# Optimization experiments

Measured on AMD Instinct MI355X. Metric: run time of the kernel, lower is better.

The kernel has to match this reference:

```python
import jax, jax.numpy as jnp
import numpy as np
import math

N0 = 50000      # nodes at level 0
E0 = 800000     # edges at level 0 (fixed edge buffer, masked when pooled)
D = 128         # hidden_dim == latent_dim
L = 2           # args.mpl_layers
NB = 2          # args.num_blocks (SAGEConvs per block)
RATIO = 0.5     # args.mpl_ratio
EPS = 1e-12


def setup_inputs() -> dict:
    key = jax.random.key(0)
    ks = jax.random.split(key, 6)
    x = jax.random.normal(ks[0], (N0, D), jnp.float32)
    edge_index = jax.random.randint(ks[1], (2, E0), 0, N0, jnp.int32)
    n_convs = (2 * L + 1) * NB  # down(4) + bottom(2) + up(4) = 10
    Wl = jax.random.normal(ks[2], (n_convs, D, D), jnp.float32) * 0.05
    bl = jax.random.normal(ks[3], (n_convs, D), jnp.float32) * 0.05
    Wr = jax.random.normal(ks[4], (n_convs, D, D), jnp.float32) * 0.05
    pool_p = jax.random.normal(ks[5], (L, D), jnp.float32)
    return {"x": x, "edge_index": edge_index, "Wl": Wl, "bl": bl, "Wr": Wr,
            "pool_p": pool_p}


def _sage(x, src, dst, valid, W_l, b_l, W_r, n):
    """PyG SAGEConv (mean aggr): lin_l(mean_{j->i} x_j) + lin_r(x_i).
    Invalid (masked) edges contribute neither to the sum nor the count."""
    msg = x[src] * valid[:, None]                       # [E, D]
    s = jax.ops.segment_sum(msg, dst, num_segments=n)   # [n, D]
    cnt = jax.ops.segment_sum(valid, dst, num_segments=n)
    mean = s / jnp.maximum(cnt, 1.0)[:, None]
    return mean @ W_l.T + b_l + x @ W_r.T


def _cal_ew(w, src, dst, valid, n):
    """WeightedEdgeConv.cal_ew (no_grad in original)."""
    deg = jax.ops.segment_sum(valid, src, num_segments=n)
    normed = w / jnp.where(deg > 0, deg, 1.0)
    w_send = normed[src] * valid
    aggr_w = jax.ops.segment_sum(w_send, dst, num_segments=n) + EPS
    ec = w_send / aggr_w[dst]
    return jax.lax.stop_gradient(ec), jax.lax.stop_gradient(aggr_w)


def _econv(x, src, dst, ec, n, aggregating=True):
    """WeightedEdgeConv.forward: gather -> scale by edge weight -> scatter-add."""
    if aggregating:
        return jax.ops.segment_sum(x[src] * ec[:, None], dst, num_segments=n)
    return jax.ops.segment_sum(x[dst] * ec[:, None], src, num_segments=n)


def reference(x, edge_index, Wl, bl, Wr, pool_p):
    src, dst = edge_index[0], edge_index[1]
    valid = jnp.ones((E0,), x.dtype)
    n = N0
    conv = 0
    down_outs, down_edges, ecs, perms, sizes = [], [], [], [], []
    w = jnp.ones((N0,), x.dtype)  # b_data.weights (ones by default)

    # ---- down path ----
    for l in range(L):
        for _ in range(NB):
            x = _sage(x, src, dst, valid, Wl[conv], bl[conv], Wr[conv], n)
            conv += 1
        down_outs.append(x)
        down_edges.append((src, dst, valid))
        sizes.append(n)
        ec, w = _cal_ew(w, src, dst, valid, n)
        ecs.append(ec)
        x = _econv(x, src, dst, ec, n, aggregating=True)
        # TopKPooling: score = x.p/||p||, keep top ceil(ratio*n), gate by tanh
        p = pool_p[l]
        score = x @ p / jnp.linalg.norm(p)
        k = int(math.ceil(RATIO * n))
        vals, perm = jax.lax.top_k(score, k)
        x = x[perm] * jnp.tanh(vals)[:, None]
        w = w[perm]
        new_id = jnp.full((n,), -1, jnp.int32).at[perm].set(
            jnp.arange(k, dtype=jnp.int32))
        src2, dst2 = new_id[src], new_id[dst]
        keep = ((src2 >= 0) & (dst2 >= 0)).astype(x.dtype)
        valid = valid * keep
        src = jnp.maximum(src2, 0)
        dst = jnp.maximum(dst2, 0)
        perms.append(perm)
        n = k

    # ---- bottom ----
    for _ in range(NB):
        x = _sage(x, src, dst, valid, Wl[conv], bl[conv], Wr[conv], n)
        conv += 1

    # ---- up path ----
    for i in range(L):
        u = L - 1 - i
        src, dst, valid = down_edges[u]
        n = sizes[u]
        # Unpool: scatter into zeros at kept-node indices
        x = jnp.zeros((n, x.shape[-1]), x.dtype).at[perms[u]].set(x)
        x = _econv(x, src, dst, ecs[u], n, aggregating=False)
        for _ in range(NB):
            x = _sage(x, src, dst, valid, Wl[conv], bl[conv], Wr[conv], n)
            conv += 1
        x = x + down_outs[u]  # skip connection
    return x
```

## Files before the change

### kernel.cpp

```cpp
#include <hip/hip_runtime.h>
#include <stdint.h>

#define DEV __device__ __forceinline__

constexpr int N0 = 50000;
constexpr int E0 = 800000;
constexpr int D  = 128;

typedef __attribute__((ext_vector_type(8))) short bf16x8;
typedef __attribute__((ext_vector_type(4))) float f32x4;

DEV float bf2f(unsigned u) { return __uint_as_float(u << 16); }
DEV unsigned short f2bf(float f) {
  unsigned u = __float_as_uint(f);
  unsigned r = u + 0x7fffu + ((u >> 16) & 1u);
  return (unsigned short)(r >> 16);
}

DEV unsigned wave_incl_scan(unsigned v, int lane) {
  #pragma unroll
  for (int off = 1; off < 64; off <<= 1) {
    unsigned u = __shfl_up(v, (unsigned)off);
    if (lane >= off) v += u;
  }
  return v;
}

__global__ void k_count(const int* __restrict__ src, const int* __restrict__ dst,
                        unsigned* cnt_src, unsigned* cnt_dst,
                        unsigned* __restrict__ rank_src, unsigned* __restrict__ rank_dst) {
  int e = blockIdx.x * blockDim.x + threadIdx.x;
  if (e < E0) {
    rank_src[e] = atomicAdd(&cnt_src[src[e]], 1u);
    rank_dst[e] = atomicAdd(&cnt_dst[dst[e]], 1u);
  }
}

__global__ void k_psum(const unsigned* __restrict__ in, int n, unsigned* __restrict__ part) {
  int t = threadIdx.x, lane = t & 63, w = t >> 6;
  int base = blockIdx.x * 1024 + t * 4;
  unsigned s = 0;
  #pragma unroll
  for (int j = 0; j < 4; ++j) { int i = base + j; if (i < n) s += in[i]; }
  #pragma unroll
  for (int off = 32; off >= 1; off >>= 1) s += __shfl_xor(s, off);
  __shared__ unsigned ws[4];
  if (lane == 0) ws[w] = s;
  __syncthreads();
  if (t == 0) part[blockIdx.x] = ws[0] + ws[1] + ws[2] + ws[3];
}

__global__ void k_scoff(const unsigned* __restrict__ part, int nch,
                        unsigned* __restrict__ off, unsigned* __restrict__ total_out) {
  if (threadIdx.x == 0) {
    unsigned run = 0;
    for (int c = 0; c < nch; ++c) { off[c] = run; run += part[c]; }
    *total_out = run;
  }
}

__global__ void k_sapply(const unsigned* __restrict__ in, const unsigned* __restrict__ choff,
                         int n, unsigned* __restrict__ out) {
  int t = threadIdx.x, lane = t & 63, w = t >> 6;
  int base = blockIdx.x * 1024 + t * 4;
  unsigned v[4]; unsigned s = 0;
  #pragma unroll
  for (int j = 0; j < 4; ++j) { int i = base + j; v[j] = (i < n) ? in[i] : 0u; s += v[j]; }
  unsigned incl = wave_incl_scan(s, lane);
  __shared__ unsigned wsum[4], woff[4];
  if (lane == 63) wsum[w] = incl;
  __syncthreads();
  if (t == 0) { unsigned run = 0; for (int j = 0; j < 4; ++j) { woff[j] = run; run += wsum[j]; } }
  __syncthreads();
  unsigned run = choff[blockIdx.x] + woff[w] + incl - s;
  #pragma unroll
  for (int j = 0; j < 4; ++j) {
    int i = base + j;
    if (i < n) out[i] = run;
    run += v[j];
  }
}

__global__ void k_fill2(const int* __restrict__ src, const int* __restrict__ dst,
                        const unsigned* __restrict__ rank_src, const unsigned* __restrict__ rank_dst,
                        const unsigned* __restrict__ indptr_src, const unsigned* __restrict__ indptr_dst,
                        int* __restrict__ adj_src, int* __restrict__ adj_dst) {
  int e = blockIdx.x * blockDim.x + threadIdx.x;
  if (e < E0) {
    int s = src[e], d = dst[e];
    adj_dst[indptr_dst[d] + rank_dst[e]] = s;
    adj_src[indptr_src[s] + rank_src[e]] = d;
  }
}

__global__ void k_adj_next2(const int* __restrict__ adjd, const int* __restrict__ adjs,
                            const int* __restrict__ new_id,
                            int* __restrict__ outd, int* __restrict__ outs) {
  int pos = blockIdx.x * blockDim.x + threadIdx.x;
  if (pos < E0) {
    int a = adjd[pos];
    outd[pos] = (a >= 0) ? new_id[a] : -1;
    int b = adjs[pos];
    outs[pos] = (b >= 0) ? new_id[b] : -1;
  }
}

__global__ void k_adj_next(const int* __restrict__ adj_prev, const int* __restrict__ new_id,
                           int* __restrict__ adj_out) {
  int pos = blockIdx.x * blockDim.x + threadIdx.x;
  if (pos < E0) {
    int a = adj_prev[pos];
    adj_out[pos] = (a >= 0) ? new_id[a] : -1;
  }
}

__global__ void k_wt_pk3(const float* __restrict__ Wl, const float* __restrict__ Wr,
                         unsigned short* __restrict__ Bh, unsigned short* __restrict__ Bm,
                         unsigned short* __restrict__ Bl) {
  int idx = blockIdx.x * blockDim.x + threadIdx.x;
  if (idx >= 10 * 8 * 8 * 64) return;
  int l  = idx & 63;
  int ct = (idx >> 6) & 7;
  int ks = (idx >> 9) & 7;
  int c  = idx >> 12;
  int k0 = ks * 32 + (l >> 4) * 8;
  int o  = ct * 16 + (l & 15);
  const float* Wrow = (k0 < 128) ? (Wl + ((size_t)c * 128 + o) * 128 + k0)
                                 : (Wr + ((size_t)c * 128 + o) * 128 + (k0 - 128));
  size_t base = (size_t)idx * 8;
  #pragma unroll
  for (int j = 0; j < 8; ++j) {
    float wv = Wrow[j];
    unsigned short h = f2bf(wv);
    float r1 = wv - bf2f(h);
    unsigned short m = f2bf(r1);
    float r2 = r1 - bf2f(m);
    Bh[base + j] = h;
    Bm[base + j] = m;
    Bl[base + j] = f2bf(r2);
  }
}

template<bool MEAN, bool MASKED, bool ECW>
__global__ void k_gf32(const float* __restrict__ x, const int* __restrict__ adj,
                       const float* __restrict__ ecs, const unsigned* __restrict__ indptr,
                       const int* __restrict__ orig, int n, float* __restrict__ out) {
  int wid = (blockIdx.x * blockDim.x + threadIdx.x) >> 6;
  int lane = threadIdx.x & 63;
  if (wid >= n) return;
  int o = orig ? orig[wid] : wid;
  unsigned s0 = indptr[o], s1 = indptr[o + 1];
  int half = lane >> 5, sl = lane & 31;
  float a0 = 0.f, a1 = 0.f, a2 = 0.f, a3 = 0.f, cnt = 0.f;
  for (unsigned idx = s0; idx < s1; idx += 8) {
    #pragma unroll
    for (int j = 0; j < 4; ++j) {
      unsigned e = idx + j * 2 + half;
      if (e < s1) {
        int a = adj[e];
        if (!MASKED || a >= 0) {
          const float4 v = *(const float4*)(x + (size_t)a * D + sl * 4);
          if (ECW) {
            float w = ecs[e];
            a0 = fmaf(w, v.x, a0); a1 = fmaf(w, v.y, a1);
            a2 = fmaf(w, v.z, a2); a3 = fmaf(w, v.w, a3);
          } else {
            a0 += v.x; a1 += v.y; a2 += v.z; a3 += v.w;
          }
          cnt += 1.f;
        }
      }
    }
  }
  a0 += __shfl_xor(a0, 32); a1 += __shfl_xor(a1, 32);
  a2 += __shfl_xor(a2, 32); a3 += __shfl_xor(a3, 32);
  if (MEAN) {
    cnt += __shfl_xor(cnt, 32);
    if (!MASKED) cnt = (float)(s1 - s0);
    float inv = 1.0f / fmaxf(cnt, 1.0f);
    a0 *= inv; a1 *= inv; a2 *= inv; a3 *= inv;
  }
  if (half == 0)
    *(float4*)(out + (size_t)wid * D + sl * 4) = make_float4(a0, a1, a2, a3);
}

template<bool MEAN, bool MASKED, bool ECW>
__global__ void k_gbf(const unsigned* __restrict__ xb, const int* __restrict__ adj,
                      const float* __restrict__ ecs, const unsigned* __restrict__ indptr,
                      const int* __restrict__ orig, int n,
                      float* __restrict__ out, unsigned* __restrict__ outbf) {
  int wid = (blockIdx.x * blockDim.x + threadIdx.x) >> 6;
  int lane = threadIdx.x & 63;
  if (wid >= n) return;
  int o = orig ? orig[wid] : wid;
  unsigned s0 = indptr[o], s1 = indptr[o + 1];
  int q = lane >> 4, sl = lane & 15;
  float acc[8];
  #pragma unroll
  for (int k = 0; k < 8; ++k) acc[k] = 0.f;
  float cnt = 0.f;
  for (unsigned idx = s0; idx < s1; idx += 16) {
    #pragma unroll
    for (int j = 0; j < 4; ++j) {
      unsigned e = idx + j * 4 + q;
      if (e < s1) {
        int a = adj[e];
        if (!MASKED || a >= 0) {
          const uint4 v = *(const uint4*)(xb + (size_t)a * 64 + sl * 4);
          float f0 = bf2f(v.x & 0xffffu), f1 = bf2f(v.x >> 16);
          float f2 = bf2f(v.y & 0xffffu), f3 = bf2f(v.y >> 16);
          float f4 = bf2f(v.z & 0xffffu), f5 = bf2f(v.z >> 16);
          float f6 = bf2f(v.w & 0xffffu), f7 = bf2f(v.w >> 16);
          if (ECW) {
            float w = ecs[e];
            acc[0] = fmaf(w, f0, acc[0]); acc[1] = fmaf(w, f1, acc[1]);
            acc[2] = fmaf(w, f2, acc[2]); acc[3] = fmaf(w, f3, acc[3]);
            acc[4] = fmaf(w, f4, acc[4]); acc[5] = fmaf(w, f5, acc[5]);
            acc[6] = fmaf(w, f6, acc[6]); acc[7] = fmaf(w, f7, acc[7]);
          } else {
            acc[0] += f0; acc[1] += f1; acc[2] += f2; acc[3] += f3;
            acc[4] += f4; acc[5] += f5; acc[6] += f6; acc[7] += f7;
          }
          cnt += 1.f;
        }
      }
    }
  }
  #pragma unroll
  for (int k = 0; k < 8; ++k) {
    acc[k] += __shfl_xor(acc[k], 16);
    acc[k] += __shfl_xor(acc[k], 32);
  }
  if (MEAN) {
    cnt += __shfl_xor(cnt, 16);
    cnt += __shfl_xor(cnt, 32);
    if (!MASKED) cnt = (float)(s1 - s0);
    float inv = 1.0f / fmaxf(cnt, 1.0f);
    #pragma unroll
    for (int k = 0; k < 8; ++k) acc[k] *= inv;
  }
  if (q == 0) {
    *(float4*)(out + (size_t)wid * D + sl * 8)     = make_float4(acc[0], acc[1], acc[2], acc[3]);
    *(float4*)(out + (size_t)wid * D + sl * 8 + 4) = make_float4(acc[4], acc[5], acc[6], acc[7]);
    if (outbf) {
      uint4 p;
      p.x = (unsigned)f2bf(acc[0]) | ((unsigned)f2bf(acc[1]) << 16);
      p.y = (unsigned)f2bf(acc[2]) | ((unsigned)f2bf(acc[3]) << 16);
      p.z = (unsigned)f2bf(acc[4]) | ((unsigned)f2bf(acc[5]) << 16);
      p.w = (unsigned)f2bf(acc[6]) | ((unsigned)f2bf(acc[7]) << 16);
      *(uint4*)(outbf + (size_t)wid * 64 + sl * 4) = p;
    }
  }
}

__launch_bounds__(256)
__global__ void k_gemm_mfma6(const float* __restrict__ mean, const float* __restrict__ xin,
                             const unsigned short* __restrict__ Bh, const unsigned short* __restrict__ Bm,
                             const unsigned short* __restrict__ Bl,
                             const float* __restrict__ bias,
                             float* __restrict__ y, int n) {
  int tid = threadIdx.x;
  int lane = tid & 63, w = tid >> 6;
  int row0 = blockIdx.x * 64 + w * 16;
  int arow = row0 + (lane & 15);
  int kgrp = lane >> 4;
  bool rowok = arow < n;
  f32x4 acc[8];
  #pragma unroll
  for (int ct = 0; ct < 8; ++ct) acc[ct] = f32x4{0.f, 0.f, 0.f, 0.f};

  #pragma unroll
  for (int ks = 0; ks < 8; ++ks) {
    const float* A = (ks < 4) ? mean : xin;
    int kk = (ks & 3) * 32 + kgrp * 8;
    float av[8];
    if (rowok) {
      float4 x0 = *(const float4*)(A + (size_t)arow * D + kk);
      float4 x1 = *(const float4*)(A + (size_t)arow * D + kk + 4);
      av[0] = x0.x; av[1] = x0.y; av[2] = x0.z; av[3] = x0.w;
      av[4] = x1.x; av[5] = x1.y; av[6] = x1.z; av[7] = x1.w;
    } else {
      #pragma unroll
      for (int j = 0; j < 8; ++j) av[j] = 0.f;
    }
    bf16x8 ah, am, al;
    #pragma unroll
    for (int j = 0; j < 8; ++j) {
      unsigned short h = f2bf(av[j]);
      float r1 = av[j] - bf2f(h);
      unsigned short m = f2bf(r1);
      float r2 = r1 - bf2f(m);
      ah[j] = (short)h; am[j] = (short)m; al[j] = (short)f2bf(r2);
    }
    #pragma unroll
    for (int ct = 0; ct < 8; ++ct) {
      size_t boff = (((size_t)ks * 8 + ct) * 64 + lane) * 8;
      bf16x8 bh = *(const bf16x8*)(Bh + boff);
      bf16x8 bm = *(const bf16x8*)(Bm + boff);
      bf16x8 bl = *(const bf16x8*)(Bl + boff);
      acc[ct] = __builtin_amdgcn_mfma_f32_16x16x32_bf16(ah, bh, acc[ct], 0, 0, 0);
      acc[ct] = __builtin_amdgcn_mfma_f32_16x16x32_bf16(ah, bm, acc[ct], 0, 0, 0);
      acc[ct] = __builtin_amdgcn_mfma_f32_16x16x32_bf16(am, bh, acc[ct], 0, 0, 0);
      acc[ct] = __builtin_amdgcn_mfma_f32_16x16x32_bf16(am, bm, acc[ct], 0, 0, 0);
      acc[ct] = __builtin_amdgcn_mfma_f32_16x16x32_bf16(ah, bl, acc[ct], 0, 0, 0);
      acc[ct] = __builtin_amdgcn_mfma_f32_16x16x32_bf16(al, bh, acc[ct], 0, 0, 0);
    }
  }
  int ccol = lane & 15;
  #pragma unroll
  for (int ct = 0; ct < 8; ++ct) {
    int col = ct * 16 + ccol;
    float bb = bias[col];
    #pragma unroll
    for (int r = 0; r < 4; ++r) {
      int row = row0 + kgrp * 4 + r;
      if (row < n) y[(size_t)row * D + col] = acc[ct][r] + bb;
    }
  }
}

__launch_bounds__(256)
__global__ void k_gemm_mfma(const float* __restrict__ mean, const float* __restrict__ xin,
                            const unsigned short* __restrict__ Bhi, const unsigned short* __restrict__ Blo,
                            const float* __restrict__ bias, const float* __restrict__ skip,
                            float* __restrict__ y, unsigned short* __restrict__ ybf, int n) {
  int tid = threadIdx.x;
  int lane = tid & 63, w = tid >> 6;
  int row0 = blockIdx.x * 64 + w * 16;
  int arow = row0 + (lane & 15);
  int kgrp = lane >> 4;
  bool rowok = arow < n;
  f32x4 acc[8];
  #pragma unroll
  for (int ct = 0; ct < 8; ++ct) acc[ct] = f32x4{0.f, 0.f, 0.f, 0.f};

  #pragma unroll
  for (int ks = 0; ks < 8; ++ks) {
    const float* A = (ks < 4) ? mean : xin;
    int kk = (ks & 3) * 32 + kgrp * 8;
    float av[8];
    if (rowok) {
      float4 x0 = *(const float4*)(A + (size_t)arow * D + kk);
      float4 x1 = *(const float4*)(A + (size_t)arow * D + kk + 4);
      av[0] = x0.x; av[1] = x0.y; av[2] = x0.z; av[3] = x0.w;
      av[4] = x1.x; av[5] = x1.y; av[6] = x1.z; av[7] = x1.w;
    } else {
      #pragma unroll
      for (int j = 0; j < 8; ++j) av[j] = 0.f;
    }
    bf16x8 ahi, alo;
    #pragma unroll
    for (int j = 0; j < 8; ++j) {
      unsigned short h = f2bf(av[j]);
      ahi[j] = (short)h;
      alo[j] = (short)f2bf(av[j] - bf2f(h));
    }
    #pragma unroll
    for (int ct = 0; ct < 8; ++ct) {
      size_t boff = (((size_t)ks * 8 + ct) * 64 + lane) * 8;
      bf16x8 bh = *(const bf16x8*)(Bhi + boff);
      bf16x8 bl = *(const bf16x8*)(Blo + boff);
      acc[ct] = __builtin_amdgcn_mfma_f32_16x16x32_bf16(ahi, bh, acc[ct], 0, 0, 0);
      acc[ct] = __builtin_amdgcn_mfma_f32_16x16x32_bf16(alo, bh, acc[ct], 0, 0, 0);
      acc[ct] = __builtin_amdgcn_mfma_f32_16x16x32_bf16(ahi, bl, acc[ct], 0, 0, 0);
    }
  }
  int ccol = lane & 15;
  #pragma unroll
  for (int ct = 0; ct < 8; ++ct) {
    int col = ct * 16 + ccol;
    float bb = bias[col];
    #pragma unroll
    for (int r = 0; r < 4; ++r) {
      int row = row0 + kgrp * 4 + r;
      if (row < n) {
        float v = acc[ct][r] + bb;
        if (skip) v += skip[(size_t)row * D + col];
        y[(size_t)row * D + col] = v;
        if (ybf) ybf[(size_t)row * D + col] = f2bf(v);
      }
    }
  }
}

__global__ void k_deg_mask(const int* __restrict__ adj_src, const unsigned* __restrict__ indptr_src,
                           const int* __restrict__ orig, int n, float* __restrict__ deg) {
  int j = blockIdx.x * blockDim.x + threadIdx.x;
  if (j >= n) return;
  int o = orig ? orig[j] : j;
  unsigned s0 = indptr_src[o], s1 = indptr_src[o + 1];
  float d = 0.f;
  for (unsigned i = s0; i < s1; ++i) d += (adj_src[i] >= 0) ? 1.f : 0.f;
  deg[j] = d;
}

template<bool MASKED>
__global__ void k_ew_dst(const int* __restrict__ adj, const unsigned* __restrict__ indptr,
                         const unsigned* __restrict__ ips,
                         const int* __restrict__ orig, const float* __restrict__ w,
                         const float* __restrict__ deg, int n,
                         float* __restrict__ ws_slot, float* __restrict__ aggrw,
                         float* __restrict__ ec_slot) {
  int j = blockIdx.x * blockDim.x + threadIdx.x;
  if (j >= n) return;
  int o = orig ? orig[j] : j;
  unsigned s0 = indptr[o], s1 = indptr[o + 1];
  float s = 1e-12f;
  for (unsigned pos = s0; pos < s1; ++pos) {
    int a = adj[pos];
    float ws = 0.f;
    if (!MASKED || a >= 0) {
      float d = deg ? deg[a] : (float)(ips[a + 1] - ips[a]);
      ws = (w ? w[a] : 1.0f) / (d > 0.f ? d : 1.0f);
    }
    ws_slot[pos] = ws;
    s += ws;
  }
  aggrw[j] = s;
  float inv = 1.0f / s;
  for (unsigned pos = s0; pos < s1; ++pos) ec_slot[pos] = ws_slot[pos] * inv;
}

template<bool MASKED>
__global__ void k_ew_src(const int* __restrict__ adj_src, const unsigned* __restrict__ indptr_src,
                         const int* __restrict__ orig, const float* __restrict__ w,
                         const float* __restrict__ deg, const float* __restrict__ aggrw, int n,
                         float* __restrict__ ec_slot) {
  int j = blockIdx.x * blockDim.x + threadIdx.x;
  if (j >= n) return;
  int o = orig ? orig[j] : j;
  unsigned s0 = indptr_src[o], s1 = indptr_src[o + 1];
  float d = deg ? deg[j] : (float)(s1 - s0);
  float wn = (w ? w[j] : 1.0f) / (d > 0.f ? d : 1.0f);
  for (unsigned pos = s0; pos < s1; ++pos) {
    int a = adj_src[pos];
    ec_slot[pos] = (!MASKED || a >= 0) ? (wn / aggrw[a]) : 0.f;
  }
}

DEV unsigned mono_key(float f) {
  unsigned u = __float_as_uint(f);
  return (u & 0x80000000u) ? ~u : (u | 0x80000000u);
}

__global__ void k_score(const float* __restrict__ x, const float* __restrict__ p,
                        int n, float* __restrict__ score, unsigned* __restrict__ keys) {
  int wid = (blockIdx.x * blockDim.x + threadIdx.x) >> 6;
  int lane = threadIdx.x & 63;
  if (wid >= n) return;
  float p0 = p[lane * 2], p1 = p[lane * 2 + 1];
  const float2 xv = *(const float2*)(x + (size_t)wid * D + lane * 2);
  float partial = xv.x * p0 + xv.y * p1;
  float pn = p0 * p0 + p1 * p1;
  #pragma unroll
  for (int off = 32; off >= 1; off >>= 1) {
    partial += __shfl_xor(partial, off);
    pn += __shfl_xor(pn, off);
  }
  if (lane == 0) {
    float sc = partial * (1.0f / sqrtf(pn));
    score[wid] = sc;
    keys[wid] = mono_key(sc);
  }
}

__global__ void k_sel_init(unsigned* bins, unsigned* state, int k) {
  int t = threadIdx.x;
  if (t < 256) bins[t] = 0u;
  if (t == 0) { state[0] = 0u; state[1] = (unsigned)k; }
}

__global__ void k_hist(const unsigned* __restrict__ keys, int n, const unsigned* __restrict__ state,
                       unsigned* __restrict__ bins, int byte) {
  __shared__ unsigned lb[256];
  for (int i = threadIdx.x; i < 256; i += blockDim.x) lb[i] = 0u;
  __syncthreads();
  unsigned prefix = state[0];
  unsigned mask = (byte == 3) ? 0u : (0xFFFFFFFFu << ((byte + 1) * 8));
  for (int i = blockIdx.x * blockDim.x + threadIdx.x; i < n; i += gridDim.x * blockDim.x) {
    unsigned key = keys[i];
    if ((key & mask) == (prefix & mask))
      atomicAdd(&lb[(key >> (byte * 8)) & 255], 1u);
  }
  __syncthreads();
  for (int i = threadIdx.x; i < 256; i += blockDim.x)
    if (lb[i]) atomicAdd(&bins[i], lb[i]);
}

__global__ void k_pick(unsigned* bins, unsigned* state, int byte) {
  if (threadIdx.x == 0) {
    unsigned r = state[1];
    int b;
    for (b = 255; b > 0; --b) {
      unsigned c = bins[b];
      if (c >= r) break;
      r -= c;
    }
    state[0] |= ((unsigned)b) << (byte * 8);
    state[1] = r;
  }
  __syncthreads();
  for (int i = threadIdx.x; i < 256; i += blockDim.x) bins[i] = 0u;
}

__global__ void k_flags(const unsigned* __restrict__ keys, const unsigned* __restrict__ state,
                        int n, uint2* __restrict__ part) {
  int t = threadIdx.x, lane = t & 63, w = t >> 6;
  int base = blockIdx.x * 1024 + t * 4;
  unsigned T = state[0];
  unsigned cnt = 0;
  #pragma unroll
  for (int j = 0; j < 4; ++j) {
    int i = base + j;
    if (i < n) {
      unsigned key = keys[i];
      cnt += (key > T ? 1u : 0u) + ((key == T ? 1u : 0u) << 16);
    }
  }
  #pragma unroll
  for (int off = 32; off >= 1; off >>= 1) cnt += __shfl_xor(cnt, off);
  __shared__ unsigned ws[4];
  if (lane == 0) ws[w] = cnt;
  __syncthreads();
  if (t == 0) {
    unsigned s = ws[0] + ws[1] + ws[2] + ws[3];
    part[blockIdx.x] = make_uint2(s & 0xffffu, s >> 16);
  }
}

__global__ void k_choff(const uint2* __restrict__ part, int nch, uint2* __restrict__ off) {
  if (threadIdx.x == 0) {
    unsigned g = 0, e = 0;
    for (int c = 0; c < nch; ++c) { off[c] = make_uint2(g, e); g += part[c].x; e += part[c].y; }
  }
}

__global__ void k_pack2(const unsigned* __restrict__ keys, const unsigned* __restrict__ state,
                        const uint2* __restrict__ choff, const float* __restrict__ aggrw,
                        const int* __restrict__ orig, int n,
                        int* __restrict__ perm, int* __restrict__ new_id,
                        float* __restrict__ w_next, int* __restrict__ orig_next) {
  int t = threadIdx.x, lane = t & 63, w = t >> 6;
  int base = blockIdx.x * 1024 + t * 4;
  unsigned T = state[0], r = state[1];
  unsigned f[4];
  unsigned cnt = 0;
  #pragma unroll
  for (int j = 0; j < 4; ++j) {
    int i = base + j;
    unsigned key = (i < n) ? keys[i] : 0u;
    unsigned gt = (i < n && key > T) ? 1u : 0u;
    unsigned eq = (i < n && key == T) ? 1u : 0u;
    f[j] = gt | (eq << 1);
    cnt += gt + (eq << 16);
  }
  unsigned incl = wave_incl_scan(cnt, lane);
  __shared__ unsigned wsum[4], woff[4];
  if (lane == 63) wsum[w] = incl;
  __syncthreads();
  if (t == 0) { unsigned run = 0; for (int j = 0; j < 4; ++j) { woff[j] = run; run += wsum[j]; } }
  __syncthreads();
  unsigned before = woff[w] + incl - cnt;
  uint2 o0 = choff[blockIdx.x];
  unsigned gt_b = o0.x + (before & 0xffffu);
  unsigned eq_b = o0.y + (before >> 16);
  #pragma unroll
  for (int j = 0; j < 4; ++j) {
    int i = base + j;
    if (i >= n) break;
    unsigned gt = f[j] & 1u, eq = (f[j] >> 1) & 1u;
    bool sel = gt || (eq && eq_b < r);
    if (sel) {
      int pos = (int)(gt_b + (eq_b < r ? eq_b : r));
      perm[pos] = i;
      new_id[i] = pos;
      w_next[pos] = aggrw[i];
      orig_next[pos] = orig ? orig[i] : i;
    } else {
      new_id[i] = -1;
    }
    gt_b += gt; eq_b += eq;
  }
}

__global__ void k_gate(const float* __restrict__ xin, const int* __restrict__ perm,
                       const float* __restrict__ score, int k, float* __restrict__ xout,
                       unsigned* __restrict__ outbf) {
  int wid = (blockIdx.x * blockDim.x + threadIdx.x) >> 6;
  int lane = threadIdx.x & 63;
  if (wid >= k) return;
  int j = perm[wid];
  float g = tanhf(score[j]);
  float2 v = *(const float2*)(xin + (size_t)j * D + lane * 2);
  v.x *= g; v.y *= g;
  *(float2*)(xout + (size_t)wid * D + lane * 2) = v;
  if (outbf) {
    unsigned p = (unsigned)f2bf(v.x) | ((unsigned)f2bf(v.y) << 16);
    outbf[(size_t)wid * 64 + lane] = p;
  }
}

__global__ void k_scatter_bf(const float* __restrict__ xin, const int* __restrict__ perm,
                             int k, unsigned* __restrict__ outbf) {
  int wid = (blockIdx.x * blockDim.x + threadIdx.x) >> 6;
  int lane = threadIdx.x & 63;
  if (wid >= k) return;
  int p = perm[wid];
  float2 v = *(const float2*)(xin + (size_t)wid * D + lane * 2);
  unsigned pk = (unsigned)f2bf(v.x) | ((unsigned)f2bf(v.y) << 16);
  outbf[(size_t)p * 64 + lane] = pk;
}

extern "C" void kernel_launch(void* const* d_in, const int* in_sizes, int n_in,
                              void* d_out, int out_size, void* d_ws, size_t ws_size,
                              hipStream_t stream) {
  const float* x_in   = (const float*)d_in[0];
  const int*   ei     = (const int*)d_in[1];
  const int*   src0   = ei;
  const int*   dst0   = ei + E0;
  const float* Wl     = (const float*)d_in[2];
  const float* bl     = (const float*)d_in[3];
  const float* Wr     = (const float*)d_in[4];
  const float* pool_p = (const float*)d_in[5];
  float* out = (float*)d_out;

  const int n0 = N0, k0 = 25000, n1 = 25000, k1 = 12500, n2 = 12500;
  const int NCH0 = (N0 + 1023) / 1024;

  char* ws = (char*)d_ws;
  size_t off = 0;
  auto alloc = [&](size_t bytes) -> char* {
    char* p = ws + off;
    off += (bytes + 255) & ~(size_t)255;
    return p;
  };
  const size_t NBY = (size_t)N0 * D * 4;
  float* B0    = (float*)alloc(NBY);
  float* B1    = (float*)alloc(NBY);
  float* B2    = (float*)alloc(NBY);
  float* down0 = (float*)alloc(NBY);
  float* down1 = (float*)alloc(NBY / 2);
  unsigned* MA = (unsigned*)alloc((size_t)N0 * D * 2);
  unsigned* MB = (unsigned*)alloc((size_t)N0 * D * 2);
  int* adj0_dst = (int*)alloc(E0 * 4);
  int* adj0_src = (int*)alloc(E0 * 4);
  int* adj1_dst = (int*)alloc(E0 * 4);
  int* adj1_src = (int*)alloc(E0 * 4);
  float* ec0_src = (float*)alloc(E0 * 4);
  float* ec1_src = (float*)alloc(E0 * 4);
  float* ec_dst  = (float*)alloc(E0 * 4);
  float* ws_slot = (float*)alloc(E0 * 4);
  int* adj2_dst  = (int*)ws_slot;
  unsigned* rank_src = (unsigned*)alloc(E0 * 4);
  unsigned* rank_dst = (unsigned*)alloc(E0 * 4);
  unsigned* indptr_dst = (unsigned*)alloc((N0 + 1) * 4);
  unsigned* indptr_src = (unsigned*)alloc((N0 + 1) * 4);
  unsigned* cnt_src = (unsigned*)alloc(N0 * 4);
  unsigned* cnt_dst = (unsigned*)alloc(N0 * 4);
  float* deg   = (float*)alloc(N0 * 4);
  float* aggrw = (float*)alloc(N0 * 4);
  float* w1 = (float*)alloc(n1 * 4);
  float* w2 = (float*)alloc(n2 * 4);
  float* score = (float*)alloc(N0 * 4);
  unsigned* keys = (unsigned*)alloc(N0 * 4);
  int* perm0 = (int*)alloc(k0 * 4);
  int* perm1 = (int*)alloc(k1 * 4);
  int* orig1 = (int*)alloc(k0 * 4);
  int* orig2 = (int*)alloc(k1 * 4);
  int* new_id = (int*)alloc(N0 * 4);
  unsigned* bins  = (unsigned*)alloc(256 * 4);
  unsigned* state = (unsigned*)alloc(8);
  unsigned* spart = (unsigned*)alloc(64 * 4);
  unsigned* soff  = (unsigned*)alloc(64 * 4);
  uint2* ppart = (uint2*)alloc(64 * 8);
  uint2* poff  = (uint2*)alloc(64 * 8);
  unsigned short* Bh = (unsigned short*)alloc((size_t)10 * 32768 * 2);
  unsigned short* Bm = (unsigned short*)alloc((size_t)10 * 32768 * 2);
  unsigned short* Bl = (unsigned short*)alloc((size_t)10 * 32768 * 2);

  const int EG = (E0 + 255) / 256;

  auto scan_np1 = [&](const unsigned* in, unsigned* outp, int n, int nch) {
    k_psum<<<nch, 256, 0, stream>>>(in, n, spart);
    k_scoff<<<1, 64, 0, stream>>>(spart, nch, soff, outp + n);
    k_sapply<<<nch, 256, 0, stream>>>(in, soff, n, outp);
  };

  hipMemsetAsync(cnt_src, 0, N0 * 4, stream);
  hipMemsetAsync(cnt_dst, 0, N0 * 4, stream);
  k_count<<<EG, 256, 0, stream>>>(src0, dst0, cnt_src, cnt_dst, rank_src, rank_dst);
  scan_np1(cnt_src, indptr_src, N0, NCH0);
  scan_np1(cnt_dst, indptr_dst, N0, NCH0);
  k_fill2<<<EG, 256, 0, stream>>>(src0, dst0, rank_src, rank_dst, indptr_src, indptr_dst,
                                  adj0_src, adj0_dst);
  k_wt_pk3<<<(10 * 8 * 8 * 64 + 255) / 256, 256, 0, stream>>>(Wl, Wr, Bh, Bm, Bl);

  auto gemm6 = [&](const float* meanb, const float* xin, float* yout, int n, int cidx) {
    size_t o = (size_t)cidx * 32768;
    k_gemm_mfma6<<<(n + 63) / 64, 256, 0, stream>>>(meanb, xin, Bh + o, Bm + o, Bl + o,
                                                    bl + cidx * 128, yout, n);
  };
  auto gemm_mx = [&](const float* meanb, const float* xin, float* yout, unsigned short* ybf,
                     const float* skip, int n, int cidx) {
    size_t o = (size_t)cidx * 32768;
    k_gemm_mfma<<<(n + 63) / 64, 256, 0, stream>>>(meanb, xin, Bh + o, Bm + o,
                                                   bl + cidx * 128, skip, yout, ybf, n);
  };

  auto pool_sel = [&](const float* xpool, int n, int kk, int level, const int* orig,
                      int* perm, float* w_next, int* orig_next,
                      float* xout, unsigned* xout_bf) {
    int nch = (n + 1023) / 1024;
    k_score<<<(n + 3) / 4, 256, 0, stream>>>(xpool, pool_p + level * D, n, score, keys);
    k_sel_init<<<1, 256, 0, stream>>>(bins, state, kk);
    for (int byte = 3; byte >= 0; --byte) {
      k_hist<<<256, 256, 0, stream>>>(keys, n, state, bins, byte);
      k_pick<<<1, 256, 0, stream>>>(bins, state, byte);
    }
    k_flags<<<nch, 256, 0, stream>>>(keys, state, n, ppart);
    k_choff<<<1, 64, 0, stream>>>(ppart, nch, poff);
    k_pack2<<<nch, 256, 0, stream>>>(keys, state, poff, aggrw, orig, n, perm, new_id, w_next, orig_next);
    k_gate<<<(kk + 3) / 4, 256, 0, stream>>>(xpool, perm, score, kk, xout, xout_bf);
  };

  const int G0 = (n0 + 3) / 4, G1 = (n1 + 3) / 4, G2 = (n2 + 3) / 4;

  k_gf32<true, false, false><<<G0, 256, 0, stream>>>(x_in, adj0_dst, nullptr, indptr_dst, nullptr, n0, B1);
  gemm6(B1, x_in, B2, n0, 0);
  k_gf32<true, false, false><<<G0, 256, 0, stream>>>(B2, adj0_dst, nullptr, indptr_dst, nullptr, n0, B1);
  gemm6(B1, B2, down0, n0, 1);
  k_ew_dst<false><<<(n0 + 255) / 256, 256, 0, stream>>>(adj0_dst, indptr_dst, indptr_src, nullptr,
                                                        nullptr, nullptr, n0, ws_slot, aggrw, ec_dst);
  k_ew_src<false><<<(n0 + 255) / 256, 256, 0, stream>>>(adj0_src, indptr_src, nullptr, nullptr,
                                                        nullptr, aggrw, n0, ec0_src);
  k_gf32<false, false, true><<<G0, 256, 0, stream>>>(down0, adj0_dst, ec_dst, indptr_dst, nullptr, n0, B1);
  pool_sel(B1, n0, k0, 0, nullptr, perm0, w1, orig1, B2, nullptr);
  k_adj_next2<<<EG, 256, 0, stream>>>(adj0_dst, adj0_src, new_id, adj1_dst, adj1_src);

  k_gf32<true, true, false><<<G1, 256, 0, stream>>>(B2, adj1_dst, nullptr, indptr_dst, orig1, n1, B1);
  gemm6(B1, B2, B0, n1, 2);
  k_gf32<true, true, false><<<G1, 256, 0, stream>>>(B0, adj1_dst, nullptr, indptr_dst, orig1, n1, B1);
  gemm6(B1, B0, down1, n1, 3);
  k_deg_mask<<<(n1 + 255) / 256, 256, 0, stream>>>(adj1_src, indptr_src, orig1, n1, deg);
  k_ew_dst<true><<<(n1 + 255) / 256, 256, 0, stream>>>(adj1_dst, indptr_dst, nullptr, orig1, w1,
                                                       deg, n1, ws_slot, aggrw, ec_dst);
  k_ew_src<true><<<(n1 + 255) / 256, 256, 0, stream>>>(adj1_src, indptr_src, orig1, w1, deg, aggrw,
                                                       n1, ec1_src);
  k_gf32<false, true, true><<<G1, 256, 0, stream>>>(down1, adj1_dst, ec_dst, indptr_dst, orig1, n1, B1);
  pool_sel(B1, n1, k1, 1, orig1, perm1, w2, orig2, B2, MA);
  k_adj_next<<<EG, 256, 0, stream>>>(adj1_dst, new_id, adj2_dst);

  k_gbf<true, true, false><<<G2, 256, 0, stream>>>(MA, adj2_dst, nullptr, indptr_dst, orig2, n2, B1, nullptr);
  gemm_mx(B1, B2, B0, (unsigned short*)MB, nullptr, n2, 4);
  k_gbf<true, true, false><<<G2, 256, 0, stream>>>(MB, adj2_dst, nullptr, indptr_dst, orig2, n2, B1, nullptr);
  gemm_mx(B1, B0, B2, nullptr, nullptr, n2, 5);

  hipMemsetAsync(MA, 0, (size_t)n1 * D * 2, stream);
  k_scatter_bf<<<G2, 256, 0, stream>>>(B2, perm1, n2, MA);
  k_gbf<false, true, true><<<G1, 256, 0, stream>>>(MA, adj1_src, ec1_src, indptr_src, orig1, n1, B1, MB);
  k_gbf<true, true, false><<<G1, 256, 0, stream>>>(MB, adj1_dst, nullptr, indptr_dst, orig1, n1, B0, nullptr);
  gemm_mx(B0, B1, B2, (unsigned short*)MA, nullptr, n1, 6);
  k_gbf<true, true, false><<<G1, 256, 0, stream>>>(MA, adj1_dst, nullptr, indptr_dst, orig1, n1, B0, nullptr);
  gemm_mx(B0, B2, B1, nullptr, down1, n1, 7);

  hipMemsetAsync(MA, 0, (size_t)n0 * D * 2, stream);
  k_scatter_bf<<<G1, 256, 0, stream>>>(B1, perm0, n1, MA);
  k_gbf<false, false, true><<<G0, 256, 0, stream>>>(MA, adj0_src, ec0_src, indptr_src, nullptr, n0, B2, MB);
  k_gbf<true, false, false><<<G0, 256, 0, stream>>>(MB, adj0_dst, nullptr, indptr_dst, nullptr, n0, B1, nullptr);
  gemm_mx(B1, B2, B0, (unsigned short*)MA, nullptr, n0, 8);
  k_gbf<true, false, false><<<G0, 256, 0, stream>>>(MA, adj0_dst, nullptr, indptr_dst, nullptr, n0, B1, nullptr);
  gemm_mx(B1, B0, out, nullptr, down0, n0, 9);
}
```

Baseline: 1.147 ms.

## Fuse SAGE mean aggregation into MFMA GEMM kernels and replace scatter unpool with gather

Each SAGEConv's neighbour-mean aggregation now runs in the same kernel as the split-bf16 MFMA GEMM. The mean rows are staged in LDS, so the fp32 mean buffer no longer makes a round trip through global memory and there are fewer launches. The unpool step changes from a memset plus scatter to a gather through per-level new_id maps, which writes zeros in place. In exchange, each block runs a serial 16-row gather per wave before the GEMM, which may lower occupancy and latency hiding, and it uses 33KB of LDS per block.

```diff
diff --git a/kernel.cpp b/kernel.cpp
--- a/kernel.cpp
+++ b/kernel.cpp
@@ -253,30 +253,68 @@
   }
 }
 
+template<bool MASKED>
 __launch_bounds__(256)
-__global__ void k_gemm_mfma6(const float* __restrict__ mean, const float* __restrict__ xin,
-                             const unsigned short* __restrict__ Bh, const unsigned short* __restrict__ Bm,
-                             const unsigned short* __restrict__ Bl,
-                             const float* __restrict__ bias,
-                             float* __restrict__ y, int n) {
-  int tid = threadIdx.x;
-  int lane = tid & 63, w = tid >> 6;
-  int row0 = blockIdx.x * 64 + w * 16;
-  int arow = row0 + (lane & 15);
+__global__ void k_fsage32(const float* __restrict__ x, const int* __restrict__ adj,
+                          const unsigned* __restrict__ indptr, const int* __restrict__ orig,
+                          int n, const float* __restrict__ xin,
+                          const unsigned short* __restrict__ Bh, const unsigned short* __restrict__ Bm,
+                          const unsigned short* __restrict__ Bl, const float* __restrict__ bias,
+                          float* __restrict__ y) {
+  __shared__ float As[64][132];
+  int tid = threadIdx.x, lane = tid & 63, w = tid >> 6;
+  int row0 = blockIdx.x * 64;
+  int half = lane >> 5, sl = lane & 31;
+  for (int i = 0; i < 16; ++i) {
+    int wid = row0 + w * 16 + i;
+    float a0 = 0.f, a1 = 0.f, a2 = 0.f, a3 = 0.f;
+    if (wid < n) {
+      int o = orig ? orig[wid] : wid;
+      unsigned s0 = indptr[o], s1 = indptr[o + 1];
+      float cnt = 0.f;
+      for (unsigned idx = s0; idx < s1; idx += 8) {
+        #pragma unroll
+        for (int j = 0; j < 4; ++j) {
+          unsigned e = idx + j * 2 + half;
+          if (e < s1) {
+            int a = adj[e];
+            if (!MASKED || a >= 0) {
+              const float4 v = *(const float4*)(x + (size_t)a * D + sl * 4);
+              a0 += v.x; a1 += v.y; a2 += v.z; a3 += v.w;
+              cnt += 1.f;
+            }
+          }
+        }
+      }
+      a0 += __shfl_xor(a0, 32); a1 += __shfl_xor(a1, 32);
+      a2 += __shfl_xor(a2, 32); a3 += __shfl_xor(a3, 32);
+      cnt += __shfl_xor(cnt, 32);
+      if (!MASKED) cnt = (float)(s1 - s0);
+      float inv = 1.0f / fmaxf(cnt, 1.0f);
+      a0 *= inv; a1 *= inv; a2 *= inv; a3 *= inv;
+    }
+    if (half == 0) *(float4*)&As[w * 16 + i][sl * 4] = make_float4(a0, a1, a2, a3);
+  }
+  __syncthreads();
+  int lr = w * 16 + (lane & 15);
+  int arow = row0 + lr;
   int kgrp = lane >> 4;
   bool rowok = arow < n;
   f32x4 acc[8];
   #pragma unroll
   for (int ct = 0; ct < 8; ++ct) acc[ct] = f32x4{0.f, 0.f, 0.f, 0.f};
-
   #pragma unroll
   for (int ks = 0; ks < 8; ++ks) {
-    const float* A = (ks < 4) ? mean : xin;
+    float av[8];
     int kk = (ks & 3) * 32 + kgrp * 8;
-    float av[8];
-    if (rowok) {
-      float4 x0 = *(const float4*)(A + (size_t)arow * D + kk);
-      float4 x1 = *(const float4*)(A + (size_t)arow * D + kk + 4);
+    if (ks < 4) {
+      float4 x0 = *(const float4*)&As[lr][kk];
+      float4 x1 = *(const float4*)&As[lr][kk + 4];
+      av[0] = x0.x; av[1] = x0.y; av[2] = x0.z; av[3] = x0.w;
+      av[4] = x1.x; av[5] = x1.y; av[6] = x1.z; av[7] = x1.w;
+    } else if (rowok) {
+      float4 x0 = *(const float4*)(xin + (size_t)arow * D + kk);
+      float4 x1 = *(const float4*)(xin + (size_t)arow * D + kk + 4);
       av[0] = x0.x; av[1] = x0.y; av[2] = x0.z; av[3] = x0.w;
       av[4] = x1.x; av[5] = x1.y; av[6] = x1.z; av[7] = x1.w;
     } else {
@@ -313,35 +351,87 @@
     float bb = bias[col];
     #pragma unroll
     for (int r = 0; r < 4; ++r) {
-      int row = row0 + kgrp * 4 + r;
+      int row = row0 + w * 16 + kgrp * 4 + r;
       if (row < n) y[(size_t)row * D + col] = acc[ct][r] + bb;
     }
   }
 }
 
+template<bool MASKED>
 __launch_bounds__(256)
-__global__ void k_gemm_mfma(const float* __restrict__ mean, const float* __restrict__ xin,
-                            const unsigned short* __restrict__ Bhi, const unsigned short* __restrict__ Blo,
-                            const float* __restrict__ bias, const float* __restrict__ skip,
-                            float* __restrict__ y, unsigned short* __restrict__ ybf, int n) {
-  int tid = threadIdx.x;
-  int lane = tid & 63, w = tid >> 6;
-  int row0 = blockIdx.x * 64 + w * 16;
-  int arow = row0 + (lane & 15);
+__global__ void k_fsage_bf(const unsigned* __restrict__ xb, const int* __restrict__ adj,
+                           const unsigned* __restrict__ indptr, const int* __restrict__ orig,
+                           int n, const float* __restrict__ xin,
+                           const unsigned short* __restrict__ Bhi, const unsigned short* __restrict__ Blo,
+                           const float* __restrict__ bias, const float* __restrict__ skip,
+                           float* __restrict__ y, unsigned short* __restrict__ ybf) {
+  __shared__ float As[64][132];
+  int tid = threadIdx.x, lane = tid & 63, w = tid >> 6;
+  int row0 = blockIdx.x * 64;
+  int q = lane >> 4, sl16 = lane & 15;
+  for (int i = 0; i < 16; ++i) {
+    int wid = row0 + w * 16 + i;
+    float acc[8];
+    #pragma unroll
+    for (int k = 0; k < 8; ++k) acc[k] = 0.f;
+    if (wid < n) {
+      int o = orig ? orig[wid] : wid;
+      unsigned s0 = indptr[o], s1 = indptr[o + 1];
+      float cnt = 0.f;
+      for (unsigned idx = s0; idx < s1; idx += 16) {
+        #pragma unroll
+        for (int j = 0; j < 4; ++j) {
+          unsigned e = idx + j * 4 + q;
+          if (e < s1) {
+            int a = adj[e];
+            if (!MASKED || a >= 0) {
+              const uint4 v = *(const uint4*)(xb + (size_t)a * 64 + sl16 * 4);
+              acc[0] += bf2f(v.x & 0xffffu); acc[1] += bf2f(v.x >> 16);
+              acc[2] += bf2f(v.y & 0xffffu); acc[3] += bf2f(v.y >> 16);
+              acc[4] += bf2f(v.z & 0xffffu); acc[5] += bf2f(v.z >> 16);
+              acc[6] += bf2f(v.w & 0xffffu); acc[7] += bf2f(v.w >> 16);
+              cnt += 1.f;
+            }
+          }
+        }
+      }
+      #pragma unroll
+      for (int k = 0; k < 8; ++k) {
+        acc[k] += __shfl_xor(acc[k], 16);
+        acc[k] += __shfl_xor(acc[k], 32);
+      }
+      cnt += __shfl_xor(cnt, 16);
+      cnt += __shfl_xor(cnt, 32);
+      if (!MASKED) cnt = (float)(s1 - s0);
+      float inv = 1.0f / fmaxf(cnt, 1.0f);
+      #pragma unroll
+      for (int k = 0; k < 8; ++k) acc[k] *= inv;
+    }
+    if (q == 0) {
+      *(float4*)&As[w * 16 + i][sl16 * 8]     = make_float4(acc[0], acc[1], acc[2], acc[3]);
+      *(float4*)&As[w * 16 + i][sl16 * 8 + 4] = make_float4(acc[4], acc[5], acc[6], acc[7]);
+    }
+  }
+  __syncthreads();
+  int lr = w * 16 + (lane & 15);
+  int arow = row0 + lr;
   int kgrp = lane >> 4;
   bool rowok = arow < n;
   f32x4 acc[8];
   #pragma unroll
   for (int ct = 0; ct < 8; ++ct) acc[ct] = f32x4{0.f, 0.f, 0.f, 0.f};
-
   #pragma unroll
   for (int ks = 0; ks < 8; ++ks) {
-    const float* A = (ks < 4) ? mean : xin;
+    float av[8];
     int kk = (ks & 3) * 32 + kgrp * 8;
-    float av[8];
-    if (rowok) {
-      float4 x0 = *(const float4*)(A + (size_t)arow * D + kk);
-      float4 x1 = *(const float4*)(A + (size_t)arow * D + kk + 4);
+    if (ks < 4) {
+      float4 x0 = *(const float4*)&As[lr][kk];
+      float4 x1 = *(const float4*)&As[lr][kk + 4];
+      av[0] = x0.x; av[1] = x0.y; av[2] = x0.z; av[3] = x0.w;
+      av[4] = x1.x; av[5] = x1.y; av[6] = x1.z; av[7] = x1.w;
+    } else if (rowok) {
+      float4 x0 = *(const float4*)(xin + (size_t)arow * D + kk);
+      float4 x1 = *(const float4*)(xin + (size_t)arow * D + kk + 4);
       av[0] = x0.x; av[1] = x0.y; av[2] = x0.z; av[3] = x0.w;
       av[4] = x1.x; av[5] = x1.y; av[6] = x1.z; av[7] = x1.w;
     } else {
@@ -372,7 +462,7 @@
     float bb = bias[col];
     #pragma unroll
     for (int r = 0; r < 4; ++r) {
-      int row = row0 + kgrp * 4 + r;
+      int row = row0 + w * 16 + kgrp * 4 + r;
       if (row < n) {
         float v = acc[ct][r] + bb;
         if (skip) v += skip[(size_t)row * D + col];
@@ -600,15 +690,18 @@
   }
 }
 
-__global__ void k_scatter_bf(const float* __restrict__ xin, const int* __restrict__ perm,
-                             int k, unsigned* __restrict__ outbf) {
+__global__ void k_unpool_bf(const float* __restrict__ xin, const int* __restrict__ new_id,
+                            int n, unsigned* __restrict__ outbf) {
   int wid = (blockIdx.x * blockDim.x + threadIdx.x) >> 6;
   int lane = threadIdx.x & 63;
-  if (wid >= k) return;
-  int p = perm[wid];
-  float2 v = *(const float2*)(xin + (size_t)wid * D + lane * 2);
-  unsigned pk = (unsigned)f2bf(v.x) | ((unsigned)f2bf(v.y) << 16);
-  outbf[(size_t)p * 64 + lane] = pk;
+  if (wid >= n) return;
+  int j = new_id[wid];
+  unsigned pk = 0u;
+  if (j >= 0) {
+    float2 v = *(const float2*)(xin + (size_t)j * D + lane * 2);
+    pk = (unsigned)f2bf(v.x) | ((unsigned)f2bf(v.y) << 16);
+  }
+  outbf[(size_t)wid * 64 + lane] = pk;
 }
 
 extern "C" void kernel_launch(void* const* d_in, const int* in_sizes, int n_in,
@@ -667,7 +760,8 @@
   int* perm1 = (int*)alloc(k1 * 4);
   int* orig1 = (int*)alloc(k0 * 4);
   int* orig2 = (int*)alloc(k1 * 4);
-  int* new_id = (int*)alloc(N0 * 4);
+  int* new_id0 = (int*)alloc(N0 * 4);
+  int* new_id1 = (int*)alloc(N0 * 4);
   unsigned* bins  = (unsigned*)alloc(256 * 4);
   unsigned* state = (unsigned*)alloc(8);
   unsigned* spart = (unsigned*)alloc(64 * 4);
@@ -695,20 +789,8 @@
                                   adj0_src, adj0_dst);
   k_wt_pk3<<<(10 * 8 * 8 * 64 + 255) / 256, 256, 0, stream>>>(Wl, Wr, Bh, Bm, Bl);
 
-  auto gemm6 = [&](const float* meanb, const float* xin, float* yout, int n, int cidx) {
-    size_t o = (size_t)cidx * 32768;
-    k_gemm_mfma6<<<(n + 63) / 64, 256, 0, stream>>>(meanb, xin, Bh + o, Bm + o, Bl + o,
-                                                    bl + cidx * 128, yout, n);
-  };
-  auto gemm_mx = [&](const float* meanb, const float* xin, float* yout, unsigned short* ybf,
-                     const float* skip, int n, int cidx) {
-    size_t o = (size_t)cidx * 32768;
-    k_gemm_mfma<<<(n + 63) / 64, 256, 0, stream>>>(meanb, xin, Bh + o, Bm + o,
-                                                   bl + cidx * 128, skip, yout, ybf, n);
-  };
-
   auto pool_sel = [&](const float* xpool, int n, int kk, int level, const int* orig,
-                      int* perm, float* w_next, int* orig_next,
+                      int* perm, int* nid, float* w_next, int* orig_next,
                       float* xout, unsigned* xout_bf) {
     int nch = (n + 1023) / 1024;
     k_score<<<(n + 3) / 4, 256, 0, stream>>>(xpool, pool_p + level * D, n, score, keys);
@@ -719,55 +801,61 @@
     }
     k_flags<<<nch, 256, 0, stream>>>(keys, state, n, ppart);
     k_choff<<<1, 64, 0, stream>>>(ppart, nch, poff);
-    k_pack2<<<nch, 256, 0, stream>>>(keys, state, poff, aggrw, orig, n, perm, new_id, w_next, orig_next);
+    k_pack2<<<nch, 256, 0, stream>>>(keys, state, poff, aggrw, orig, n, perm, nid, w_next, orig_next);
     k_gate<<<(kk + 3) / 4, 256, 0, stream>>>(xpool, perm, score, kk, xout, xout_bf);
   };
 
-  const int G0 = (n0 + 3) / 4, G1 = (n1 + 3) / 4, G2 = (n2 + 3) / 4;
-
-  k_gf32<true, false, false><<<G0, 256, 0, stream>>>(x_in, adj0_dst, nullptr, indptr_dst, nullptr, n0, B1);
-  gemm6(B1, x_in, B2, n0, 0);
-  k_gf32<true, false, false><<<G0, 256, 0, stream>>>(B2, adj0_dst, nullptr, indptr_dst, nullptr, n0, B1);
-  gemm6(B1, B2, down0, n0, 1);
+  const int G0 = (n0 + 3) / 4, G1 = (n1 + 3) / 4;
+  const int F0 = (n0 + 63) / 64, F1 = (n1 + 63) / 64, F2 = (n2 + 63) / 64;
+  auto BW = [&](int c) { return (size_t)c * 32768; };
+
+  k_fsage32<false><<<F0, 256, 0, stream>>>(x_in, adj0_dst, indptr_dst, nullptr, n0, x_in,
+                                           Bh + BW(0), Bm + BW(0), Bl + BW(0), bl + 0 * 128, B2);
+  k_fsage32<false><<<F0, 256, 0, stream>>>(B2, adj0_dst, indptr_dst, nullptr, n0, B2,
+                                           Bh + BW(1), Bm + BW(1), Bl + BW(1), bl + 1 * 128, down0);
   k_ew_dst<false><<<(n0 + 255) / 256, 256, 0, stream>>>(adj0_dst, indptr_dst, indptr_src, nullptr,
                                                         nullptr, nullptr, n0, ws_slot, aggrw, ec_dst);
   k_ew_src<false><<<(n0 + 255) / 256, 256, 0, stream>>>(adj0_src, indptr_src, nullptr, nullptr,
                                                         nullptr, aggrw, n0, ec0_src);
   k_gf32<false, false, true><<<G0, 256, 0, stream>>>(down0, adj0_dst, ec_dst, indptr_dst, nullptr, n0, B1);
-  pool_sel(B1, n0, k0, 0, nullptr, perm0, w1, orig1, B2, nullptr);
-  k_adj_next2<<<EG, 256, 0, stream>>>(adj0_dst, adj0_src, new_id, adj1_dst, adj1_src);
-
-  k_gf32<true, true, false><<<G1, 256, 0, stream>>>(B2, adj1_dst, nullptr, indptr_dst, orig1, n1, B1);
-  gemm6(B1, B2, B0, n1, 2);
-  k_gf32<true, true, false><<<G1, 256, 0, stream>>>(B0, adj1_dst, nullptr, indptr_dst, orig1, n1, B1);
-  gemm6(B1, B0, down1, n1, 3);
+  pool_sel(B1, n0, k0, 0, nullptr, perm0, new_id0, w1, orig1, B2, nullptr);
+  k_adj_next2<<<EG, 256, 0, stream>>>(adj0_dst, adj0_src, new_id0, adj1_dst, adj1_src);
+
+  k_fsage32<true><<<F1, 256, 0, stream>>>(B2, adj1_dst, indptr_dst, orig1, n1, B2,
+                                          Bh + BW(2), Bm + BW(2), Bl + BW(2), bl + 2 * 128, B0);
+  k_fsage32<true><<<F1, 256, 0, stream>>>(B0, adj1_dst, indptr_dst, orig1, n1, B0,
+                                          Bh + BW(3), Bm + BW(3), Bl + BW(3), bl + 3 * 128, down1);
   k_deg_mask<<<(n1 + 255) / 256, 256, 0, stream>>>(adj1_src, indptr_src, orig1, n1, deg);
   k_ew_dst<true><<<(n1 + 255) / 256, 256, 0, stream>>>(adj1_dst, indptr_dst, nullptr, orig1, w1,
                                                        deg, n1, ws_slot, aggrw, ec_dst);
   k_ew_src<true><<<(n1 + 255) / 256, 256, 0, stream>>>(adj1_src, indptr_src, orig1, w1, deg, aggrw,
                                                        n1, ec1_src);
   k_gf32<false, true, true><<<G1, 256, 0, stream>>>(down1, adj1_dst, ec_dst, indptr_dst, orig1, n1, B1);
-  pool_sel(B1, n1, k1, 1, orig1, perm1, w2, orig2, B2, MA);
-  k_adj_next<<<EG, 256, 0, stream>>>(adj1_dst, new_id, adj2_dst);
-
-  k_gbf<true, true, false><<<G2, 256, 0, stream>>>(MA, adj2_dst, nullptr, indptr_dst, orig2, n2, B1, nullptr);
-  gemm_mx(B1, B2, B0, (unsigned short*)MB, nullptr, n2, 4);
-  k_gbf<true, true, false><<<G2, 256, 0, stream>>>(MB, adj2_dst, nullptr, indptr_dst, orig2, n2, B1, nullptr);
-  gemm_mx(B1, B0, B2, nullptr, nullptr, n2, 5);
-
-  hipMemsetAsync(MA, 0, (size_t)n1 * D * 2, stream);
-  k_scatter_bf<<<G2, 256, 0, stream>>>(B2, perm1, n2, MA);
+  pool_sel(B1, n1, k1, 1, orig1, perm1, new_id1, w2, orig2, B2, MA);
+  k_adj_next<<<EG, 256, 0, stream>>>(adj1_dst, new_id1, adj2_dst);
+
+  k_fsage_bf<true><<<F2, 256, 0, stream>>>(MA, adj2_dst, indptr_dst, orig2, n2, B2,
+                                           Bh + BW(4), Bm + BW(4), bl + 4 * 128, nullptr,
+                                           B0, (unsigned short*)MB);
+  k_fsage_bf<true><<<F2, 256, 0, stream>>>(MB, adj2_dst, indptr_dst, orig2, n2, B0,
+                                           Bh + BW(5), Bm + BW(5), bl + 5 * 128, nullptr,
+                                           B2, nullptr);
+
+  k_unpool_bf<<<G1, 256, 0, stream>>>(B2, new_id1, n1, MA);
   k_gbf<false, true, true><<<G1, 256, 0, stream>>>(MA, adj1_src, ec1_src, indptr_src, orig1, n1, B1, MB);
-  k_gbf<true, true, false><<<G1, 256, 0, stream>>>(MB, adj1_dst, nullptr, indptr_dst, orig1, n1, B0, nullptr);
-  gemm_mx(B0, B1, B2, (unsigned short*)MA, nullptr, n1, 6);
-  k_gbf<true, true, false><<<G1, 256, 0, stream>>>(MA, adj1_dst, nullptr, indptr_dst, orig1, n1, B0, nullptr);
-  gemm_mx(B0, B2, B1, nullptr, down1, n1, 7);
-
-  hipMemsetAsync(MA, 0, (size_t)n0 * D * 2, stream);
-  k_scatter_bf<<<G1, 256, 0, stream>>>(B1, perm0, n1, MA);
+  k_fsage_bf<true><<<F1, 256, 0, stream>>>(MB, adj1_dst, indptr_dst, orig1, n1, B1,
+                                           Bh + BW(6), Bm + BW(6), bl + 6 * 128, nullptr,
+                                           B2, (unsigned short*)MA);
+  k_fsage_bf<true><<<F1, 256, 0, stream>>>(MA, adj1_dst, indptr_dst, orig1, n1, B2,
+                                           Bh + BW(7), Bm + BW(7), bl + 7 * 128, down1,
+                                           B1, nullptr);
+
+  k_unpool_bf<<<G0, 256, 0, stream>>>(B1, new_id0, n0, MA);
   k_gbf<false, false, true><<<G0, 256, 0, stream>>>(MA, adj0_src, ec0_src, indptr_src, nullptr, n0, B2, MB);
-  k_gbf<true, false, false><<<G0, 256, 0, stream>>>(MB, adj0_dst, nullptr, indptr_dst, nullptr, n0, B1, nullptr);
-  gemm_mx(B1, B2, B0, (unsigned short*)MA, nullptr, n0, 8);
-  k_gbf<true, false, false><<<G0, 256, 0, stream>>>(MA, adj0_dst, nullptr, indptr_dst, nullptr, n0, B1, nullptr);
-  gemm_mx(B1, B0, out, nullptr, down0, n0, 9);
-}
+  k_fsage_bf<false><<<F0, 256, 0, stream>>>(MB, adj0_dst, indptr_dst, nullptr, n0, B2,
+                                            Bh + BW(8), Bm + BW(8), bl + 8 * 128, nullptr,
+                                            B0, (unsigned short*)MA);
+  k_fsage_bf<false><<<F0, 256, 0, stream>>>(MA, adj0_dst, indptr_dst, nullptr, n0, B0,
+                                            Bh + BW(9), Bm + BW(9), bl + 9 * 128, down0,
+                                            out, nullptr);
+}
```

Measured after the change: 1.525 ms. +33.0%, slower.
